# Kernel optimization log

Hardware: AMD Instinct MI355X
Metric: run time of the kernel (lower is better)

## Reference

```python
import jax, jax.numpy as jnp
import numpy as np

B, S, E = 1, 4096, 2048
H, KVH, HD = 16, 4, 128
WIN = 2048  # sliding window size
ROPE_BASE = 10000.0


def setup_inputs() -> dict:
    rng = jax.random.key(0)
    ks = jax.random.split(rng, 7)
    s = 0.02
    return {
        "query": jax.random.normal(ks[0], (B, S, E), jnp.float32),
        "key": jax.random.normal(ks[1], (B, S, E), jnp.float32),
        "value": jax.random.normal(ks[2], (B, S, E), jnp.float32),
        "position_ids": jnp.broadcast_to(jnp.arange(S, dtype=jnp.int64), (B, S)),
        "wq": jax.random.normal(ks[3], (E, H * HD), jnp.float32) * s,
        "wk": jax.random.normal(ks[4], (E, KVH * HD), jnp.float32) * s,
        "wv": jax.random.normal(ks[5], (E, KVH * HD), jnp.float32) * s,
        "wo": jax.random.normal(ks[6], (H * HD, E), jnp.float32) * s,
    }


def _rotate_half(x):
    x1, x2 = x[..., : HD // 2], x[..., HD // 2 :]
    return jnp.concatenate([-x2, x1], axis=-1)


def reference(query, key, value, position_ids, wq, wk, wv, wo):
    # projections (nn.Linear, no bias)
    q = (query @ wq).reshape(B, S, H, HD).transpose(0, 2, 1, 3)     # [B,H,S,D]
    k = (key @ wk).reshape(B, S, KVH, HD).transpose(0, 2, 1, 3)     # [B,KVH,S,D]
    v = (value @ wv).reshape(B, S, KVH, HD).transpose(0, 2, 1, 3)

    # RoPE (MistralRotaryEmbedding + apply_rotary_pos_emb)
    inv_freq = 1.0 / (ROPE_BASE ** (jnp.arange(0, HD, 2, dtype=jnp.float32) / HD))
    ang = position_ids.astype(jnp.float32)[..., None] * inv_freq   # [B,S,D/2]
    emb = jnp.concatenate([ang, ang], axis=-1)                      # [B,S,D]
    cos = jnp.cos(emb)[:, None]                                     # [B,1,S,D]
    sin = jnp.sin(emb)[:, None]
    q = q * cos + _rotate_half(q) * sin
    k = k * cos + _rotate_half(k) * sin

    # GQA: repeat_kv
    n_rep = H // KVH
    k = jnp.repeat(k, n_rep, axis=1)                                # [B,H,S,D]
    v = jnp.repeat(v, n_rep, axis=1)

    scale = 1.0 / np.sqrt(HD).astype(np.float32)
    scores = jnp.einsum("bhqd,bhkd->bhqk", q, k) * scale            # [B,H,S,S]
    i = jnp.arange(S)[:, None]
    j = jnp.arange(S)[None, :]
    mask = (j <= i) & (j >= i - WIN)                                # causal, window left
    scores = jnp.where(mask, scores, jnp.finfo(scores.dtype).min)
    attn = jax.nn.softmax(scores, axis=-1)
    out = jnp.einsum("bhqk,bhkd->bhqd", attn, v)                    # [B,H,S,D]
    out = out.transpose(0, 2, 1, 3).reshape(B, S, H * HD)
    return out @ wo
```

## Files before the change

### kernel.cpp

```cpp
#include <hip/hip_runtime.h>
#include <hip/hip_bf16.h>
#include <cmath>

typedef __bf16 bf16;
typedef bf16 bf16x4 __attribute__((ext_vector_type(4)));
typedef float f32x4 __attribute__((ext_vector_type(4)));
typedef short short8 __attribute__((ext_vector_type(8)));

#define S_LEN 4096
#define EMB   2048
#define NH    16
#define NKV   4
#define HD    128
#define WIN   2048

__global__ __launch_bounds__(256)
void cvt_f32_bf16(const float* __restrict__ X, bf16* __restrict__ Y)
{
    long i = ((long)blockIdx.x * 256 + threadIdx.x) * 8;
    f32x4 a = *(const f32x4*)(X + i);
    f32x4 b = *(const f32x4*)(X + i + 4);
    short8 v;
    #pragma unroll
    for (int k = 0; k < 4; k++) {
        ((bf16*)&v)[k]     = (bf16)a[k];
        ((bf16*)&v)[4 + k] = (bf16)b[k];
    }
    *(short8*)(Y + i) = v;
}

__global__ __launch_bounds__(256)
void transpose_w(const float* __restrict__ W, bf16* __restrict__ Wt, int K, int N)
{
    __shared__ float t[32][33];
    const int k0 = blockIdx.x * 32, n0 = blockIdx.y * 32;
    const int tx = threadIdx.x & 31, ty = threadIdx.x >> 5;
    #pragma unroll
    for (int i = 0; i < 4; i++)
        t[ty + 8 * i][tx] = W[(long)(k0 + ty + 8 * i) * N + n0 + tx];
    __syncthreads();
    #pragma unroll
    for (int i = 0; i < 4; i++)
        Wt[(long)(n0 + ty + 8 * i) * K + k0 + tx] = (bf16)t[tx][ty + 8 * i];
}

template<bool A_BF16, bool C_BF16>
__global__ __launch_bounds__(256)
void gemm_mfma(const void* __restrict__ Ap, const bf16* __restrict__ Bt,
               void* __restrict__ Cp, int M, int N, int K)
{
    __shared__ __align__(16) bf16 As[128 * 32];
    __shared__ __align__(16) bf16 Bs[128 * 32];
    char* AsB = (char*)As;
    char* BsB = (char*)Bs;
    const int tid = threadIdx.x;
    const int n0 = blockIdx.x * 128, m0 = blockIdx.y * 128;
    const int w = tid >> 6;
    const int wm = (w >> 1) * 64, wn = (w & 1) * 64;
    const int l16 = tid & 15, lq4 = (tid & 63) >> 4;

    const f32x4 fz = {0.f, 0.f, 0.f, 0.f};
    f32x4 acc[4][4];
    #pragma unroll
    for (int i = 0; i < 4; i++)
        #pragma unroll
        for (int j = 0; j < 4; j++) acc[i][j] = fz;

    const int sr = tid >> 1;
    const int sh = (tid & 1) * 16;
    const long arow = (long)(m0 + sr) * K;
    const long brow = (long)(n0 + sr) * K;
    const int wbase = sr * 64;
    const int swz = (sr & 7) << 4;

    for (int k0 = 0; k0 < K; k0 += 32) {
        __syncthreads();
        short8 av0, av1;
        if (A_BF16) {
            const bf16* A = (const bf16*)Ap;
            av0 = *(const short8*)(A + arow + k0 + sh);
            av1 = *(const short8*)(A + arow + k0 + sh + 8);
        } else {
            const float* A = (const float*)Ap;
            f32x4 a0 = *(const f32x4*)(A + arow + k0 + sh);
            f32x4 a1 = *(const f32x4*)(A + arow + k0 + sh + 4);
            f32x4 a2 = *(const f32x4*)(A + arow + k0 + sh + 8);
            f32x4 a3 = *(const f32x4*)(A + arow + k0 + sh + 12);
            bf16* p0 = (bf16*)&av0;
            bf16* p1 = (bf16*)&av1;
            #pragma unroll
            for (int i = 0; i < 4; i++) {
                p0[i]     = (bf16)a0[i];
                p0[4 + i] = (bf16)a1[i];
                p1[i]     = (bf16)a2[i];
                p1[4 + i] = (bf16)a3[i];
            }
        }
        short8 bv0 = *(const short8*)(Bt + brow + k0 + sh);
        short8 bv1 = *(const short8*)(Bt + brow + k0 + sh + 8);
        *(short8*)(AsB + ((wbase + sh * 2     ) ^ swz)) = av0;
        *(short8*)(AsB + ((wbase + sh * 2 + 16) ^ swz)) = av1;
        *(short8*)(BsB + ((wbase + sh * 2     ) ^ swz)) = bv0;
        *(short8*)(BsB + ((wbase + sh * 2 + 16) ^ swz)) = bv1;
        __syncthreads();

        short8 af[4], bfr[4];
        #pragma unroll
        for (int i = 0; i < 4; i++) {
            int mr = wm + i * 16 + l16;
            af[i]  = *(const short8*)(AsB + ((mr * 64 + lq4 * 16) ^ ((mr & 7) << 4)));
            int nr = wn + i * 16 + l16;
            bfr[i] = *(const short8*)(BsB + ((nr * 64 + lq4 * 16) ^ ((nr & 7) << 4)));
        }
        #pragma unroll
        for (int i = 0; i < 4; i++)
            #pragma unroll
            for (int j = 0; j < 4; j++)
                acc[i][j] = __builtin_amdgcn_mfma_f32_16x16x32_bf16(
                    af[i], bfr[j], acc[i][j], 0, 0, 0);
    }

    #pragma unroll
    for (int i = 0; i < 4; i++)
        #pragma unroll
        for (int r = 0; r < 4; r++) {
            long row = m0 + wm + i * 16 + lq4 * 4 + r;
            #pragma unroll
            for (int j = 0; j < 4; j++) {
                long col = n0 + wn + j * 16 + l16;
                if (C_BF16) ((bf16*)Cp)[row * N + col] = (bf16)acc[i][j][r];
                else        ((float*)Cp)[row * N + col] = acc[i][j][r];
            }
        }
}

__global__ __launch_bounds__(256)
void rope_k(bf16* __restrict__ X, int nh)
{
    int idx = blockIdx.x * 256 + threadIdx.x;
    int i = idx & 63;
    int h = (idx >> 6) % nh;
    int s = idx / (64 * nh);
    bf16* p = X + (long)s * (nh * HD) + h * HD + i;
    float x1 = (float)p[0];
    float x2 = (float)p[64];
    float f = exp2f((float)i * (-13.287712379549449f / 64.0f));
    float ang = (float)s * f;
    float sn, cs;
    sincosf(ang, &sn, &cs);
    p[0]  = (bf16)(x1 * cs - x2 * sn);
    p[64] = (bf16)(x2 * cs + x1 * sn);
}

__global__ __launch_bounds__(256)
void transpose_v(const bf16* __restrict__ V, bf16* __restrict__ Vt)
{
    __shared__ bf16 t[32][33];
    const int s0 = blockIdx.x * 32;
    const int d0 = blockIdx.y * 32;
    const int tx = threadIdx.x & 31, ty = threadIdx.x >> 5;
    #pragma unroll
    for (int k = 0; k < 4; k++)
        t[ty + 8 * k][tx] = V[(long)(s0 + ty + 8 * k) * (NKV * HD) + d0 + tx];
    __syncthreads();
    #pragma unroll
    for (int k = 0; k < 4; k++) {
        int drow = d0 + ty + 8 * k;
        Vt[(long)drow * S_LEN + s0 + tx] = t[tx][ty + 8 * k];
    }
}

__global__ __launch_bounds__(256)
void attn_mfma(const bf16* __restrict__ Qb, const bf16* __restrict__ Kb,
               const bf16* __restrict__ Vt, bf16* __restrict__ Ob)
{
    __shared__ __align__(16) bf16 Kl[64 * 128];
    __shared__ __align__(16) bf16 Vl[128 * 64];
    __shared__ __align__(16) bf16 Pl[4][16][72];

    const int qb  = (int)gridDim.x - 1 - blockIdx.x;
    const int q0  = qb * 64;
    const int h   = blockIdx.y;
    const int kvh = h >> 2;
    const int tid = threadIdx.x;
    const int w   = tid >> 6;
    const int l16 = tid & 15;
    const int lq4 = (tid & 63) >> 4;
    const int qw  = q0 + w * 16;
    const int qi  = qw + l16;

    short8 aQ[4];
    {
        const bf16* qp = Qb + (long)qi * EMB + h * HD + lq4 * 8;
        #pragma unroll
        for (int c = 0; c < 4; c++) aQ[c] = *(const short8*)(qp + c * 32);
    }

    const f32x4 fz = {0.f, 0.f, 0.f, 0.f};
    float mrow = -1e30f, lrow = 0.f;
    f32x4 accO[8];
    #pragma unroll
    for (int dt = 0; dt < 8; dt++) accO[dt] = fz;

    const int jb0 = (q0 >= WIN) ? q0 - WIN : 0;
    char* KlB = (char*)Kl;
    char* VlB = (char*)Vl;

    short8 stgK[4], stgV[4];
    #pragma unroll
    for (int it = 0; it < 4; it++) {
        int c = it * 256 + tid;
        stgK[it] = *(const short8*)(Kb + (long)(jb0 + (c >> 4)) * (NKV * HD) + kvh * HD + (c & 15) * 8);
        stgV[it] = *(const short8*)(Vt + ((long)kvh * HD + (c >> 3)) * S_LEN + jb0 + (c & 7) * 8);
    }

    for (int jb = jb0; jb <= q0; jb += 64) {
        __syncthreads();
        #pragma unroll
        for (int it = 0; it < 4; it++) {
            int c = it * 256 + tid;
            int key = c >> 4, d0 = (c & 15) * 8;
            *(short8*)(KlB + ((key * 256 + d0 * 2) ^ ((key & 7) << 4))) = stgK[it];
            int d = c >> 3, k0 = (c & 7) * 8;
            *(short8*)(VlB + ((d * 128 + k0 * 2) ^ ((d & 7) << 4))) = stgV[it];
        }
        __syncthreads();
        if (jb + 64 <= q0) {
            #pragma unroll
            for (int it = 0; it < 4; it++) {
                int c = it * 256 + tid;
                stgK[it] = *(const short8*)(Kb + (long)(jb + 64 + (c >> 4)) * (NKV * HD) + kvh * HD + (c & 15) * 8);
                stgV[it] = *(const short8*)(Vt + ((long)kvh * HD + (c >> 3)) * S_LEN + jb + 64 + (c & 7) * 8);
            }
        }

        f32x4 s[4];
        #pragma unroll
        for (int jt = 0; jt < 4; jt++) {
            const int key = jt * 16 + l16;
            f32x4 a = fz;
            #pragma unroll
            for (int c = 0; c < 4; c++) {
                short8 bk = *(const short8*)(
                    KlB + ((key * 256 + c * 64 + lq4 * 16) ^ ((key & 7) << 4)));
                a = __builtin_amdgcn_mfma_f32_16x16x32_bf16(bk, aQ[c], a, 0, 0, 0);
            }
            s[jt] = a;
        }

        float tmax = -1e30f;
        const bool need_mask = (jb == q0) || (q0 >= WIN && jb == jb0);
        if (need_mask) {
            #pragma unroll
            for (int jt = 0; jt < 4; jt++)
                #pragma unroll
                for (int r = 0; r < 4; r++) {
                    int j = jb + jt * 16 + lq4 * 4 + r;
                    float sv = s[jt][r] * 0.08838834764831845f;
                    if (j > qi || j < qi - WIN) sv = -1e30f;
                    s[jt][r] = sv;
                    tmax = fmaxf(tmax, sv);
                }
        } else {
            #pragma unroll
            for (int jt = 0; jt < 4; jt++)
                #pragma unroll
                for (int r = 0; r < 4; r++) {
                    float sv = s[jt][r] * 0.08838834764831845f;
                    s[jt][r] = sv;
                    tmax = fmaxf(tmax, sv);
                }
        }
        tmax = fmaxf(tmax, __shfl_xor(tmax, 16, 64));
        tmax = fmaxf(tmax, __shfl_xor(tmax, 32, 64));

        float mn = fmaxf(mrow, tmax);
        float alpha = __expf(mrow - mn);
        mrow = mn;
        float rsum = 0.f;
        #pragma unroll
        for (int jt = 0; jt < 4; jt++) {
            bf16x4 pb4;
            #pragma unroll
            for (int r = 0; r < 4; r++) {
                float pv = __expf(s[jt][r] - mn);
                bf16 pb = (bf16)pv;
                pb4[r] = pb;
                rsum += (float)pb;
            }
            *(bf16x4*)&Pl[w][l16][jt * 16 + lq4 * 4] = pb4;
        }
        rsum += __shfl_xor(rsum, 16, 64);
        rsum += __shfl_xor(rsum, 32, 64);
        lrow = lrow * alpha + rsum;
        #pragma unroll
        for (int dt = 0; dt < 8; dt++)
            accO[dt] *= alpha;

        #pragma unroll
        for (int kc = 0; kc < 2; kc++) {
            short8 ap = *(const short8*)&Pl[w][l16][kc * 32 + lq4 * 8];
            #pragma unroll
            for (int dt = 0; dt < 8; dt++) {
                int d = dt * 16 + l16;
                short8 bv = *(const short8*)(
                    VlB + ((d * 128 + kc * 64 + lq4 * 16) ^ ((d & 7) << 4)));
                accO[dt] = __builtin_amdgcn_mfma_f32_16x16x32_bf16(bv, ap, accO[dt], 0, 0, 0);
            }
        }
    }

    float inv = 1.0f / lrow;
    bf16* op = Ob + (long)qi * EMB + h * HD + lq4 * 4;
    #pragma unroll
    for (int dt = 0; dt < 8; dt++) {
        bf16x4 o4;
        #pragma unroll
        for (int r = 0; r < 4; r++) o4[r] = (bf16)(accO[dt][r] * inv);
        *(bf16x4*)(op + dt * 16) = o4;
    }
}

extern "C" void kernel_launch(void* const* d_in, const int* in_sizes, int n_in,
                              void* d_out, int out_size, void* d_ws, size_t ws_size,
                              hipStream_t stream)
{
    (void)out_size; (void)ws_size;
    int idx_pos = -1;
    for (int i = 0; i < n_in; i++)
        if (in_sizes[i] == 4096) { idx_pos = i; break; }
    int bigs[3] = {0, 1, 2}, w4[2] = {4, 6}, w1[2] = {5, 5};
    int nb = 0, n4 = 0, n1 = 0;
    for (int i = 0; i < n_in; i++) {
        if (in_sizes[i] == 8388608 && nb < 3) bigs[nb++] = i;
        else if (in_sizes[i] == 4194304 && n4 < 2) w4[n4++] = i;
        else if (in_sizes[i] == 1048576 && n1 < 2) w1[n1++] = i;
    }
    bool alpha = (idx_pos == 1);
    int iq  = alpha ? bigs[1] : bigs[0];
    int ik  = alpha ? bigs[0] : bigs[1];
    int iv  = bigs[2];
    int iwq = alpha ? w4[1] : w4[0];
    int iwo = alpha ? w4[0] : w4[1];
    int iwk = w1[0];
    int iwv = w1[1];
    const float* query = (const float*)d_in[iq];
    const float* key   = (const float*)d_in[ik];
    const float* value = (const float*)d_in[iv];
    const float* wq = (const float*)d_in[iwq];
    const float* wk = (const float*)d_in[iwk];
    const float* wv = (const float*)d_in[iwv];
    const float* wo = (const float*)d_in[iwo];

    bf16* Qb  = (bf16*)d_out;
    char* ws = (char*)d_ws;
    bf16* wqT = (bf16*)(ws);
    bf16* Qf  = (bf16*)(ws + (8u  << 20));
    bf16* Kb  = (bf16*)(ws);
    bf16* Vb  = (bf16*)(ws + (4u  << 20));
    bf16* Ob  = (bf16*)(ws + (8u  << 20));
    bf16* Vt  = (bf16*)(ws + (24u << 20));
    bf16* wkT = (bf16*)(ws + (24u << 20));
    bf16* wvT = (bf16*)(ws + (26u << 20));
    bf16* woT = (bf16*)(ws);

    dim3 blk(256);
    transpose_w<<<dim3(EMB / 32, EMB / 32), blk, 0, stream>>>(wq, wqT, EMB, EMB);
    cvt_f32_bf16<<<(S_LEN * EMB) / 2048, blk, 0, stream>>>(query, Qf);
    gemm_mfma<true, true><<<dim3(EMB / 128, S_LEN / 128), blk, 0, stream>>>(
        Qf, wqT, Qb, S_LEN, EMB, EMB);

    transpose_w<<<dim3(EMB / 32, (NKV * HD) / 32), blk, 0, stream>>>(wk, wkT, EMB, NKV * HD);
    transpose_w<<<dim3(EMB / 32, (NKV * HD) / 32), blk, 0, stream>>>(wv, wvT, EMB, NKV * HD);
    gemm_mfma<false, true><<<dim3((NKV * HD) / 128, S_LEN / 128), blk, 0, stream>>>(
        key, wkT, Kb, S_LEN, NKV * HD, EMB);
    gemm_mfma<false, true><<<dim3((NKV * HD) / 128, S_LEN / 128), blk, 0, stream>>>(
        value, wvT, Vb, S_LEN, NKV * HD, EMB);

    rope_k<<<(S_LEN * NH * 64) / 256, blk, 0, stream>>>(Qb, NH);
    rope_k<<<(S_LEN * NKV * 64) / 256, blk, 0, stream>>>(Kb, NKV);
    transpose_v<<<dim3(S_LEN / 32, (NKV * HD) / 32), blk, 0, stream>>>(Vb, Vt);
    attn_mfma<<<dim3(S_LEN / 64, NH), blk, 0, stream>>>(Qb, Kb, Vt, Ob);

    transpose_w<<<dim3((NH * HD) / 32, EMB / 32), blk, 0, stream>>>(wo, woT, NH * HD, EMB);
    gemm_mfma<true, false><<<dim3(EMB / 128, S_LEN / 128), blk, 0, stream>>>(
        Ob, woT, d_out, S_LEN, EMB, EMB);
}
```

Before: 617.0 us.

## Add direct global-to-LDS GEMM and lazy-rescale exp2 softmax in attention

```diff
diff --git a/kernel.cpp b/kernel.cpp
--- a/kernel.cpp
+++ b/kernel.cpp
@@ -14,6 +14,13 @@
 #define HD    128
 #define WIN   2048
 
+#define SCALE2 0.12751743f
+#define DTHR   8.0f
+
+#define GLOAD_LDS16(g, l) __builtin_amdgcn_global_load_lds( \
+    (const __attribute__((address_space(1))) void*)(g),     \
+    (__attribute__((address_space(3))) void*)(l), 16, 0, 0)
+
 __global__ __launch_bounds__(256)
 void cvt_f32_bf16(const float* __restrict__ X, bf16* __restrict__ Y)
 {
@@ -42,6 +49,73 @@
     #pragma unroll
     for (int i = 0; i < 4; i++)
         Wt[(long)(n0 + ty + 8 * i) * K + k0 + tx] = (bf16)t[tx][ty + 8 * i];
+}
+
+template<bool C_BF16>
+__global__ __launch_bounds__(256)
+void gemm_lds(const bf16* __restrict__ A, const bf16* __restrict__ Bt,
+              void* __restrict__ Cp, int M, int N, int K)
+{
+    __shared__ __align__(16) bf16 As[128 * 32];
+    __shared__ __align__(16) bf16 Bs[128 * 32];
+    char* AsB = (char*)As;
+    char* BsB = (char*)Bs;
+    const int tid  = threadIdx.x;
+    const int n0 = blockIdx.x * 128, m0 = blockIdx.y * 128;
+    const int w = tid >> 6;
+    const int lane = tid & 63;
+    const int wm = (w >> 1) * 64, wn = (w & 1) * 64;
+    const int l16 = tid & 15, lq4 = lane >> 4;
+
+    const f32x4 fz = {0.f, 0.f, 0.f, 0.f};
+    f32x4 acc[4][4];
+    #pragma unroll
+    for (int i = 0; i < 4; i++)
+        #pragma unroll
+        for (int j = 0; j < 4; j++) acc[i][j] = fz;
+
+    const int srow = w * 16 + (lane >> 2);
+    const int scol = (lane & 3) * 8;
+    const bf16* Ag = A  + (long)(m0 + srow) * K + scol;
+    const bf16* Bg = Bt + (long)(n0 + srow) * K + scol;
+    char* Al = AsB + w * 1024 + (lane & 63) * 0;
+    char* Bl = BsB + w * 1024;
+
+    for (int k0 = 0; k0 < K; k0 += 32) {
+        __syncthreads();
+        GLOAD_LDS16(Ag,            Al);
+        GLOAD_LDS16(Ag + 64 * K,   Al + 4096);
+        GLOAD_LDS16(Bg,            Bl);
+        GLOAD_LDS16(Bg + 64 * K,   Bl + 4096);
+        __syncthreads();
+        Ag += 32; Bg += 32;
+
+        short8 af[4], bfr[4];
+        #pragma unroll
+        for (int i = 0; i < 4; i++) {
+            af[i]  = *(const short8*)(AsB + (wm + i * 16 + l16) * 64 + lq4 * 16);
+            bfr[i] = *(const short8*)(BsB + (wn + i * 16 + l16) * 64 + lq4 * 16);
+        }
+        #pragma unroll
+        for (int i = 0; i < 4; i++)
+            #pragma unroll
+            for (int j = 0; j < 4; j++)
+                acc[i][j] = __builtin_amdgcn_mfma_f32_16x16x32_bf16(
+                    af[i], bfr[j], acc[i][j], 0, 0, 0);
+    }
+
+    #pragma unroll
+    for (int i = 0; i < 4; i++)
+        #pragma unroll
+        for (int r = 0; r < 4; r++) {
+            long row = m0 + wm + i * 16 + lq4 * 4 + r;
+            #pragma unroll
+            for (int j = 0; j < 4; j++) {
+                long col = n0 + wn + j * 16 + l16;
+                if (C_BF16) ((bf16*)Cp)[row * N + col] = (bf16)acc[i][j][r];
+                else        ((float*)Cp)[row * N + col] = acc[i][j][r];
+            }
+        }
 }
 
 template<bool A_BF16, bool C_BF16>
@@ -206,13 +280,17 @@
     char* KlB = (char*)Kl;
     char* VlB = (char*)Vl;
 
+    const bf16* pK = Kb + (long)(jb0 + (tid >> 4)) * (NKV * HD) + kvh * HD + (tid & 15) * 8;
+    const bf16* pV = Vt + ((long)kvh * HD + (tid >> 3)) * S_LEN + jb0 + (tid & 7) * 8;
+
     short8 stgK[4], stgV[4];
     #pragma unroll
     for (int it = 0; it < 4; it++) {
-        int c = it * 256 + tid;
-        stgK[it] = *(const short8*)(Kb + (long)(jb0 + (c >> 4)) * (NKV * HD) + kvh * HD + (c & 15) * 8);
-        stgV[it] = *(const short8*)(Vt + ((long)kvh * HD + (c >> 3)) * S_LEN + jb0 + (c & 7) * 8);
-    }
+        stgK[it] = *(const short8*)(pK + it * 16 * (NKV * HD));
+        stgV[it] = *(const short8*)(pV + it * 32 * S_LEN);
+    }
+    pK += 64 * (NKV * HD);
+    pV += 64;
 
     for (int jb = jb0; jb <= q0; jb += 64) {
         __syncthreads();
@@ -228,10 +306,11 @@
         if (jb + 64 <= q0) {
             #pragma unroll
             for (int it = 0; it < 4; it++) {
-                int c = it * 256 + tid;
-                stgK[it] = *(const short8*)(Kb + (long)(jb + 64 + (c >> 4)) * (NKV * HD) + kvh * HD + (c & 15) * 8);
-                stgV[it] = *(const short8*)(Vt + ((long)kvh * HD + (c >> 3)) * S_LEN + jb + 64 + (c & 7) * 8);
-            }
+                stgK[it] = *(const short8*)(pK + it * 16 * (NKV * HD));
+                stgV[it] = *(const short8*)(pV + it * 32 * S_LEN);
+            }
+            pK += 64 * (NKV * HD);
+            pV += 64;
         }
 
         f32x4 s[4];
@@ -256,7 +335,7 @@
                 #pragma unroll
                 for (int r = 0; r < 4; r++) {
                     int j = jb + jt * 16 + lq4 * 4 + r;
-                    float sv = s[jt][r] * 0.08838834764831845f;
+                    float sv = s[jt][r] * SCALE2;
                     if (j > qi || j < qi - WIN) sv = -1e30f;
                     s[jt][r] = sv;
                     tmax = fmaxf(tmax, sv);
@@ -266,7 +345,7 @@
             for (int jt = 0; jt < 4; jt++)
                 #pragma unroll
                 for (int r = 0; r < 4; r++) {
-                    float sv = s[jt][r] * 0.08838834764831845f;
+                    float sv = s[jt][r] * SCALE2;
                     s[jt][r] = sv;
                     tmax = fmaxf(tmax, sv);
                 }
@@ -274,16 +353,23 @@
         tmax = fmaxf(tmax, __shfl_xor(tmax, 16, 64));
         tmax = fmaxf(tmax, __shfl_xor(tmax, 32, 64));
 
-        float mn = fmaxf(mrow, tmax);
-        float alpha = __expf(mrow - mn);
-        mrow = mn;
+        if (!__all(tmax - mrow <= DTHR)) {
+            float mn = fmaxf(mrow, tmax);
+            float alpha = exp2f(mrow - mn);
+            mrow = mn;
+            lrow *= alpha;
+            #pragma unroll
+            for (int dt = 0; dt < 8; dt++)
+                accO[dt] *= alpha;
+        }
+
         float rsum = 0.f;
         #pragma unroll
         for (int jt = 0; jt < 4; jt++) {
             bf16x4 pb4;
             #pragma unroll
             for (int r = 0; r < 4; r++) {
-                float pv = __expf(s[jt][r] - mn);
+                float pv = exp2f(s[jt][r] - mrow);
                 bf16 pb = (bf16)pv;
                 pb4[r] = pb;
                 rsum += (float)pb;
@@ -292,10 +378,7 @@
         }
         rsum += __shfl_xor(rsum, 16, 64);
         rsum += __shfl_xor(rsum, 32, 64);
-        lrow = lrow * alpha + rsum;
-        #pragma unroll
-        for (int dt = 0; dt < 8; dt++)
-            accO[dt] *= alpha;
+        lrow += rsum;
 
         #pragma unroll
         for (int kc = 0; kc < 2; kc++) {
@@ -367,7 +450,7 @@
     dim3 blk(256);
     transpose_w<<<dim3(EMB / 32, EMB / 32), blk, 0, stream>>>(wq, wqT, EMB, EMB);
     cvt_f32_bf16<<<(S_LEN * EMB) / 2048, blk, 0, stream>>>(query, Qf);
-    gemm_mfma<true, true><<<dim3(EMB / 128, S_LEN / 128), blk, 0, stream>>>(
+    gemm_lds<true><<<dim3(EMB / 128, S_LEN / 128), blk, 0, stream>>>(
         Qf, wqT, Qb, S_LEN, EMB, EMB);
 
     transpose_w<<<dim3(EMB / 32, (NKV * HD) / 32), blk, 0, stream>>>(wk, wkT, EMB, NKV * HD);
@@ -383,6 +466,6 @@
     attn_mfma<<<dim3(S_LEN / 64, NH), blk, 0, stream>>>(Qb, Kb, Vt, Ob);
 
     transpose_w<<<dim3((NH * HD) / 32, EMB / 32), blk, 0, stream>>>(wo, woT, NH * HD, EMB);
-    gemm_mfma<true, false><<<dim3(EMB / 128, S_LEN / 128), blk, 0, stream>>>(
+    gemm_lds<false><<<dim3(EMB / 128, S_LEN / 128), blk, 0, stream>>>(
         Ob, woT, d_out, S_LEN, EMB, EMB);
 }
```

New measurement: 613.7 us. No clear change (-0.5%).
